# Kernel tuning notes

Measured on AMD Instinct MI355X. Metric: run time of the kernel, lower is better.

Reference implementation:

```python
import jax, jax.numpy as jnp
import numpy as np

D_MODEL = 1024
NUM_HEADS = 16
DEPTH = D_MODEL // NUM_HEADS


def setup_inputs() -> dict:
    key = jax.random.key(0)
    ks = jax.random.split(key, 8)
    B, S, D = 2, 2048, D_MODEL
    s = 1.0 / np.sqrt(D)
    return {
        "q": jax.random.normal(ks[0], (B, S, D), jnp.float32),
        "k": jax.random.normal(ks[1], (B, S, D), jnp.float32),
        "v": jax.random.normal(ks[2], (B, S, D), jnp.float32),
        "Wq": jax.random.normal(ks[3], (D, D), jnp.float32) * s,
        "bq": jnp.zeros((D,), jnp.float32),
        "Wk": jax.random.normal(ks[4], (D, D), jnp.float32) * s,
        "bk": jnp.zeros((D,), jnp.float32),
        "Wv": jax.random.normal(ks[5], (D, D), jnp.float32) * s,
        "bv": jnp.zeros((D,), jnp.float32),
        "Wo": jax.random.normal(ks[6], (D, D), jnp.float32) * s,
        "bo": jnp.zeros((D,), jnp.float32),
    }


def _split_heads(x):
    # [B,S,D] -> [B,H,S,depth]
    B, S, _ = x.shape
    return x.reshape(B, S, NUM_HEADS, DEPTH).transpose(0, 2, 1, 3)


def reference(q, k, v, Wq, bq, Wk, bk, Wv, bv, Wo, bo):
    qh = _split_heads(q @ Wq + bq)  # [B,H,S,d]
    kh = _split_heads(k @ Wk + bk)
    vh = _split_heads(v @ Wv + bv)
    scale = 1.0 / jnp.sqrt(jnp.float32(DEPTH))
    logits = jnp.einsum("bhqd,bhkd->bhqk", qh, kh) * scale  # [B,H,S,S]
    weights = jax.nn.softmax(logits, axis=-1)
    attn = jnp.einsum("bhqk,bhkd->bhqd", weights, vh)
    B, H, S, d = attn.shape
    attn = attn.transpose(0, 2, 1, 3).reshape(B, S, H * d)  # [B,S,D]
    return attn @ Wo + bo
```

## Files before the change

### kernel.cpp

```cpp
#include <hip/hip_runtime.h>
#include <hip/hip_bf16.h>
#include <stdint.h>


typedef __attribute__((ext_vector_type(8))) short bf16x8;
typedef __attribute__((ext_vector_type(4))) float f32x4;

#define MFMA16(a, b, c) __builtin_amdgcn_mfma_f32_16x16x32_bf16((a), (b), (c), 0, 0, 0)
#define EXP2(x) __builtin_amdgcn_exp2f(x)

static constexpr int S_LEN = 2048;
static constexpr int DM    = 1024;
static constexpr int DEPTH = 64;
static constexpr float QSCALE = 0.125f * 1.44269504088896340736f;

__device__ __forceinline__ unsigned short f2b(float f) {
  unsigned u = __float_as_uint(f);
  unsigned r = 0x7FFFu + ((u >> 16) & 1u);
  return (unsigned short)((u + r) >> 16);
}

__device__ __forceinline__ unsigned short b16(float f) {
  __hip_bfloat16 h = __float2bfloat16(f);
  union { __hip_bfloat16 h; unsigned short u; } c; c.h = h; return c.u;
}

__device__ __forceinline__ void gload16(const void* g, void* l) {
  __builtin_amdgcn_global_load_lds(
      (const __attribute__((address_space(1))) void*)g,
      (__attribute__((address_space(3))) void*)l, 16, 0, 0);
}

__device__ __forceinline__ void wave_lds_fence() {
  asm volatile("" ::: "memory");
  __builtin_amdgcn_sched_barrier(0);
}

__global__ __launch_bounds__(256) void prep_k(
    const float* __restrict__ xq, const float* __restrict__ xk,
    const float* __restrict__ xv, unsigned short* __restrict__ Xb,
    const float* __restrict__ Wq, const float* __restrict__ Wk,
    const float* __restrict__ Wv, const float* __restrict__ Wo,
    unsigned short* __restrict__ Wt) {
  __shared__ unsigned short ts[64][68];
  const int bid = blockIdx.x;
  const int tid = threadIdx.x;
  if (bid < 6144) {
    const int which = bid >> 11;
    const int xb = bid & 2047;
    const float* X = (which == 0) ? xq : (which == 1) ? xk : xv;
    size_t gid = ((size_t)xb * 256 + tid) * 8;
    float4 v0 = *(const float4*)&X[gid];
    float4 v1 = *(const float4*)&X[gid + 4];
    union { unsigned short u[8]; bf16x8 v; } pk;
    pk.u[0] = f2b(v0.x); pk.u[1] = f2b(v0.y); pk.u[2] = f2b(v0.z); pk.u[3] = f2b(v0.w);
    pk.u[4] = f2b(v1.x); pk.u[5] = f2b(v1.y); pk.u[6] = f2b(v1.z); pk.u[7] = f2b(v1.w);
    *(bf16x8*)&Xb[(size_t)which * 4096 * DM + gid] = pk.v;
    return;
  }
  const int wb = bid - 6144;
  const int w = wb >> 8, tile = wb & 255;
  const int tr = tile >> 4, tc = tile & 15;
  const float* W = (w == 0) ? Wq : (w == 1) ? Wk : (w == 2) ? Wv : Wo;
  unsigned short* T = Wt + (size_t)w * DM * DM;
  const int kr = tid >> 4, nc = (tid & 15) * 4;
  #pragma unroll
  for (int j = 0; j < 4; ++j) {
    int k = tr * 64 + kr + j * 16;
    float4 v = *(const float4*)&W[(size_t)k * DM + tc * 64 + nc];
    ushort4 u; u.x = f2b(v.x); u.y = f2b(v.y); u.z = f2b(v.z); u.w = f2b(v.w);
    *(ushort4*)&ts[kr + j * 16][nc] = u;
  }
  __syncthreads();
  const int nr = tid >> 4, kc = (tid & 15) * 4;
  #pragma unroll
  for (int j = 0; j < 4; ++j) {
    int n = tc * 64 + nr + j * 16;
    ushort4 u;
    u.x = ts[kc + 0][nr + j * 16];
    u.y = ts[kc + 1][nr + j * 16];
    u.z = ts[kc + 2][nr + j * 16];
    u.w = ts[kc + 3][nr + j * 16];
    *(ushort4*)&T[(size_t)n * DM + tr * 64 + kc] = u;
  }
}

__global__ __launch_bounds__(256, 4) void proj_qkv_k(
    const unsigned short* __restrict__ Xb, const unsigned short* __restrict__ Wt,
    const float* __restrict__ bq, const float* __restrict__ bk, const float* __restrict__ bv,
    unsigned short* __restrict__ Qh, unsigned short* __restrict__ Kh,
    unsigned short* __restrict__ Vt) {
  __shared__ __align__(16) unsigned short As[2][128][32];
  __shared__ __align__(16) unsigned short Bs[2][128][32];

  const int z = blockIdx.z;
  const unsigned short* A  = Xb + (size_t)z * 4096 * DM;
  const unsigned short* Bt = Wt + (size_t)z * DM * DM;
  const float* bias = (z == 0) ? bq : (z == 1) ? bk : bv;
  const float scale = (z == 0) ? QSCALE : 1.0f;
  unsigned short* O = (z == 0) ? Qh : (z == 1) ? Kh : Vt;

  const int bm = blockIdx.x, bn = blockIdx.y;
  const int tid = threadIdx.x;
  const int wave = tid >> 6, lane = tid & 63;
  const int wr = wave >> 1, wc = wave & 1;
  const int g = lane >> 4, i16 = lane & 15;
  const int srow = tid >> 2, sslot = tid & 3;

  f32x4 acc[4][4] = {};

  auto stage = [&](int ks, int buf) {
    #pragma unroll
    for (int rnd = 0; rnd < 2; ++rnd) {
      int row = rnd * 64 + srow;
      int sw = sslot ^ ((row >> 1) & 3);
      gload16(&A[(size_t)(bm * 128 + row) * DM + ks * 32 + sw * 8],
              &As[buf][row][sslot * 8]);
      gload16(&Bt[(size_t)(bn * 128 + row) * DM + ks * 32 + sw * 8],
              &Bs[buf][row][sslot * 8]);
    }
  };
  auto compute = [&](int buf) {
    bf16x8 a[4], b[4];
    #pragma unroll
    for (int m = 0; m < 4; ++m) {
      int row = wr * 64 + m * 16 + i16;
      int sl = g ^ ((row >> 1) & 3);
      a[m] = *(const bf16x8*)&As[buf][row][sl * 8];
    }
    #pragma unroll
    for (int n = 0; n < 4; ++n) {
      int row = wc * 64 + n * 16 + i16;
      int sl = g ^ ((row >> 1) & 3);
      b[n] = *(const bf16x8*)&Bs[buf][row][sl * 8];
    }
    #pragma unroll
    for (int m = 0; m < 4; ++m)
      #pragma unroll
      for (int n = 0; n < 4; ++n)
        acc[m][n] = MFMA16(a[m], b[n], acc[m][n]);
  };

  stage(0, 0);
  __syncthreads();
  int cur = 0;
  #pragma unroll 1
  for (int ks = 0; ks < DM / 32; ++ks) {
    if (ks + 1 < DM / 32) stage(ks + 1, cur ^ 1);
    compute(cur);
    __syncthreads();
    cur ^= 1;
  }

  #pragma unroll
  for (int m = 0; m < 4; ++m) {
    #pragma unroll
    for (int n = 0; n < 4; ++n) {
      #pragma unroll
      for (int r = 0; r < 4; ++r) {
        int row = bm * 128 + wr * 64 + m * 16 + g * 4 + r;
        int col = bn * 128 + wc * 64 + n * 16 + i16;
        float v = (acc[m][n][r] + bias[col]) * scale;
        int b_ = row >> 11, s = row & 2047;
        int h = col >> 6, dd = col & 63;
        if (z != 2)
          O[(((size_t)(b_ * 16 + h)) * S_LEN + s) * DEPTH + dd] = f2b(v);
        else
          O[(((size_t)(b_ * 16 + h)) * DEPTH + dd) * S_LEN + s] = f2b(v);
      }
    }
  }
}

__global__ __launch_bounds__(256, 4) void out_proj_k(
    const unsigned short* __restrict__ At, const unsigned short* __restrict__ Wto,
    const float* __restrict__ bo, float* __restrict__ out) {
  __shared__ __align__(16) unsigned short As[2][64][32];
  __shared__ __align__(16) unsigned short Bs[2][128][32];

  const int bm = blockIdx.x, bn = blockIdx.y;
  const int tid = threadIdx.x;
  const int wave = tid >> 6, lane = tid & 63;
  const int wr = wave >> 1, wc = wave & 1;
  const int g = lane >> 4, i16 = lane & 15;
  const int srow = tid >> 2, sslot = tid & 3;

  f32x4 acc[2][4] = {};

  auto stage = [&](int ks, int buf) {
    {
      int sw = sslot ^ ((srow >> 1) & 3);
      gload16(&At[(size_t)(bm * 64 + srow) * DM + ks * 32 + sw * 8],
              &As[buf][srow][sslot * 8]);
    }
    #pragma unroll
    for (int rnd = 0; rnd < 2; ++rnd) {
      int row = rnd * 64 + srow;
      int sw = sslot ^ ((row >> 1) & 3);
      gload16(&Wto[(size_t)(bn * 128 + row) * DM + ks * 32 + sw * 8],
              &Bs[buf][row][sslot * 8]);
    }
  };
  auto compute = [&](int buf) {
    bf16x8 a[2], b[4];
    #pragma unroll
    for (int m = 0; m < 2; ++m) {
      int row = wr * 32 + m * 16 + i16;
      int sl = g ^ ((row >> 1) & 3);
      a[m] = *(const bf16x8*)&As[buf][row][sl * 8];
    }
    #pragma unroll
    for (int n = 0; n < 4; ++n) {
      int row = wc * 64 + n * 16 + i16;
      int sl = g ^ ((row >> 1) & 3);
      b[n] = *(const bf16x8*)&Bs[buf][row][sl * 8];
    }
    #pragma unroll
    for (int m = 0; m < 2; ++m)
      #pragma unroll
      for (int n = 0; n < 4; ++n)
        acc[m][n] = MFMA16(a[m], b[n], acc[m][n]);
  };

  stage(0, 0);
  __syncthreads();
  int cur = 0;
  #pragma unroll 1
  for (int ks = 0; ks < DM / 32; ++ks) {
    if (ks + 1 < DM / 32) stage(ks + 1, cur ^ 1);
    compute(cur);
    __syncthreads();
    cur ^= 1;
  }

  #pragma unroll
  for (int m = 0; m < 2; ++m) {
    #pragma unroll
    for (int n = 0; n < 4; ++n) {
      #pragma unroll
      for (int r = 0; r < 4; ++r) {
        int row = bm * 64 + wr * 32 + m * 16 + g * 4 + r;
        int col = bn * 128 + wc * 64 + n * 16 + i16;
        out[(size_t)row * DM + col] = acc[m][n][r] + bo[col];
      }
    }
  }
}

__global__ __launch_bounds__(256) void attn_k(
    const unsigned short* __restrict__ Qh, const unsigned short* __restrict__ Kh,
    const unsigned short* __restrict__ Vt, unsigned short* __restrict__ Ob) {
  __shared__ unsigned short Ks[2][128][64];
  __shared__ unsigned short Vs[2][64][128];
  __shared__ unsigned short p_lds[4][2][16][64];

  const int linear = blockIdx.y * 16 + blockIdx.x;
  const int wg = (linear & 7) * 64 + (linear >> 3);
  const int qt = wg & 15, bh = wg >> 4;

  const int tid = threadIdx.x;
  const int wave = tid >> 6, lane = tid & 63;
  const int g = lane >> 4, i16 = lane & 15;

  const unsigned short* Q = Qh + (size_t)bh * S_LEN * DEPTH;
  const unsigned short* K = Kh + (size_t)bh * S_LEN * DEPTH;
  const unsigned short* V = Vt + (size_t)bh * DEPTH * S_LEN;

  const int ksr = tid >> 3, kss = tid & 7;
  const int vsr = tid >> 4, vss = tid & 15;

  const int qbase = qt * 128 + wave * 32;
  bf16x8 qa[2][2];
  #pragma unroll
  for (int qs = 0; qs < 2; ++qs) {
    qa[qs][0] = *(const bf16x8*)&Q[(size_t)(qbase + qs * 16 + i16) * DEPTH + g * 8];
    qa[qs][1] = *(const bf16x8*)&Q[(size_t)(qbase + qs * 16 + i16) * DEPTH + 32 + g * 8];
  }

  const short one_b = (short)0x3F80;
  const bf16x8 ones = {one_b, one_b, one_b, one_b, one_b, one_b, one_b, one_b};

  f32x4 l_acc[2] = {};
  f32x4 o[2][4] = {};

  auto stage = [&](int t, int buf) {
    const int kv = t * 128;
    #pragma unroll
    for (int j = 0; j < 4; ++j) {
      int kr = j * 32 + ksr;
      int ksw = kss ^ (kr & 7);
      gload16(&K[(size_t)(kv + kr) * DEPTH + ksw * 8], &Ks[buf][kr][kss * 8]);
      int vr = j * 16 + vsr;
      int vsw = vss ^ (vr & 7);
      gload16(&V[(size_t)vr * S_LEN + kv + vsw * 8], &Vs[buf][vr][vss * 8]);
    }
  };

  stage(0, 0);
  __syncthreads();

  int cur = 0;
  #pragma unroll 1
  for (int t128 = 0; t128 < 16; ++t128) {
    if (t128 + 1 < 16) stage(t128 + 1, cur ^ 1);

    #pragma unroll
    for (int h = 0; h < 2; ++h) {
      f32x4 sT[2][4];
      const f32x4 zero = {0.f, 0.f, 0.f, 0.f};
      __builtin_amdgcn_s_setprio(1);
      #pragma unroll
      for (int t = 0; t < 4; ++t) {
        int row = h * 64 + t * 16 + i16;
        int x = row & 7;
        bf16x8 k0 = *(const bf16x8*)&Ks[cur][row][(g ^ x) * 8];
        bf16x8 k1 = *(const bf16x8*)&Ks[cur][row][((4 + g) ^ x) * 8];
        #pragma unroll
        for (int qs = 0; qs < 2; ++qs) {
          f32x4 s = MFMA16(k0, qa[qs][0], zero);
          sT[qs][t] = MFMA16(k1, qa[qs][1], s);
        }
      }
      __builtin_amdgcn_s_setprio(0);

      wave_lds_fence();
      #pragma unroll
      for (int qs = 0; qs < 2; ++qs) {
        #pragma unroll
        for (int t = 0; t < 4; ++t) {
          ushort4 w;
          w.x = b16(EXP2(sT[qs][t][0]));
          w.y = b16(EXP2(sT[qs][t][1]));
          w.z = b16(EXP2(sT[qs][t][2]));
          w.w = b16(EXP2(sT[qs][t][3]));
          int idx = (((t * 2 + (g >> 1)) ^ (i16 & 7)) * 8) + (g & 1) * 4;
          *(ushort4*)&p_lds[wave][qs][i16][idx] = w;
        }
      }
      wave_lds_fence();
      bf16x8 pa0[2], pa1[2];
      #pragma unroll
      for (int qs = 0; qs < 2; ++qs) {
        pa0[qs] = *(const bf16x8*)&p_lds[wave][qs][i16][(g ^ (i16 & 7)) * 8];
        pa1[qs] = *(const bf16x8*)&p_lds[wave][qs][i16][((4 + g) ^ (i16 & 7)) * 8];
      }

      __builtin_amdgcn_s_setprio(1);
      #pragma unroll
      for (int dt = 0; dt < 4; ++dt) {
        int row = dt * 16 + i16;
        int x = row & 7;
        bf16x8 v0 = *(const bf16x8*)&Vs[cur][row][((h * 8 + g) ^ x) * 8];
        bf16x8 v1 = *(const bf16x8*)&Vs[cur][row][((h * 8 + 4 + g) ^ x) * 8];
        #pragma unroll
        for (int qs = 0; qs < 2; ++qs) {
          o[qs][dt] = MFMA16(pa0[qs], v0, o[qs][dt]);
          o[qs][dt] = MFMA16(pa1[qs], v1, o[qs][dt]);
        }
      }
      #pragma unroll
      for (int qs = 0; qs < 2; ++qs) {
        l_acc[qs] = MFMA16(pa0[qs], ones, l_acc[qs]);
        l_acc[qs] = MFMA16(pa1[qs], ones, l_acc[qs]);
      }
      __builtin_amdgcn_s_setprio(0);
    }

    __syncthreads();
    cur ^= 1;
  }

  const int b_ = bh >> 4, h_ = bh & 15;
  #pragma unroll
  for (int qs = 0; qs < 2; ++qs) {
    f32x4 rinv;
    #pragma unroll
    for (int r = 0; r < 4; ++r)
      rinv[r] = 1.0f / l_acc[qs][r];
    #pragma unroll
    for (int dt = 0; dt < 4; ++dt) {
      #pragma unroll
      for (int r = 0; r < 4; ++r) {
        int qrow = qbase + qs * 16 + g * 4 + r;
        float val = o[qs][dt][r] * rinv[r];
        Ob[((size_t)(b_ * S_LEN + qrow)) * DM + h_ * DEPTH + dt * 16 + i16] = f2b(val);
      }
    }
  }
}

extern "C" void kernel_launch(void* const* d_in, const int* in_sizes, int n_in,
                              void* d_out, int out_size, void* d_ws, size_t ws_size,
                              hipStream_t stream) {
  const float* q  = (const float*)d_in[0];
  const float* k  = (const float*)d_in[1];
  const float* v  = (const float*)d_in[2];
  const float* Wq = (const float*)d_in[3];
  const float* bq = (const float*)d_in[4];
  const float* Wk = (const float*)d_in[5];
  const float* bk = (const float*)d_in[6];
  const float* Wv = (const float*)d_in[7];
  const float* bv = (const float*)d_in[8];
  const float* Wo = (const float*)d_in[9];
  const float* bo = (const float*)d_in[10];
  float* out = (float*)d_out;

  const size_t HEAD_ELEMS = (size_t)2 * 16 * S_LEN * DEPTH;
  unsigned short* Qh = (unsigned short*)d_ws;
  unsigned short* Kh = Qh + HEAD_ELEMS;
  unsigned short* Vt = Kh + HEAD_ELEMS;
  unsigned short* Xb = Vt + HEAD_ELEMS;
  unsigned short* At = Xb;
  unsigned short* Wt = Xb + 3 * HEAD_ELEMS;

  dim3 blk(256);
  hipLaunchKernelGGL(prep_k, dim3(7168), blk, 0, stream,
                     q, k, v, Xb, Wq, Wk, Wv, Wo, Wt);
  hipLaunchKernelGGL(proj_qkv_k, dim3(32, 8, 3), blk, 0, stream,
                     Xb, Wt, bq, bk, bv, Qh, Kh, Vt);
  hipLaunchKernelGGL(attn_k, dim3(16, 32), blk, 0, stream, Qh, Kh, Vt, At);
  hipLaunchKernelGGL(out_proj_k, dim3(64, 8), blk, 0, stream,
                     At, Wt + (size_t)3 * DM * DM, bo, out);
}
```

Measured before the change: 123.7 us.

## Fuse fp32-to-bf16 activation conversion into QKV projection GEMM loads

```diff
diff --git a/kernel.cpp b/kernel.cpp
--- a/kernel.cpp
+++ b/kernel.cpp
@@ -37,29 +37,13 @@
 }
 
 __global__ __launch_bounds__(256) void prep_k(
-    const float* __restrict__ xq, const float* __restrict__ xk,
-    const float* __restrict__ xv, unsigned short* __restrict__ Xb,
     const float* __restrict__ Wq, const float* __restrict__ Wk,
     const float* __restrict__ Wv, const float* __restrict__ Wo,
     unsigned short* __restrict__ Wt) {
   __shared__ unsigned short ts[64][68];
   const int bid = blockIdx.x;
   const int tid = threadIdx.x;
-  if (bid < 6144) {
-    const int which = bid >> 11;
-    const int xb = bid & 2047;
-    const float* X = (which == 0) ? xq : (which == 1) ? xk : xv;
-    size_t gid = ((size_t)xb * 256 + tid) * 8;
-    float4 v0 = *(const float4*)&X[gid];
-    float4 v1 = *(const float4*)&X[gid + 4];
-    union { unsigned short u[8]; bf16x8 v; } pk;
-    pk.u[0] = f2b(v0.x); pk.u[1] = f2b(v0.y); pk.u[2] = f2b(v0.z); pk.u[3] = f2b(v0.w);
-    pk.u[4] = f2b(v1.x); pk.u[5] = f2b(v1.y); pk.u[6] = f2b(v1.z); pk.u[7] = f2b(v1.w);
-    *(bf16x8*)&Xb[(size_t)which * 4096 * DM + gid] = pk.v;
-    return;
-  }
-  const int wb = bid - 6144;
-  const int w = wb >> 8, tile = wb & 255;
+  const int w = bid >> 8, tile = bid & 255;
   const int tr = tile >> 4, tc = tile & 15;
   const float* W = (w == 0) ? Wq : (w == 1) ? Wk : (w == 2) ? Wv : Wo;
   unsigned short* T = Wt + (size_t)w * DM * DM;
@@ -86,15 +70,16 @@
 }
 
 __global__ __launch_bounds__(256, 4) void proj_qkv_k(
-    const unsigned short* __restrict__ Xb, const unsigned short* __restrict__ Wt,
+    const float* __restrict__ xq, const float* __restrict__ xk,
+    const float* __restrict__ xv, const unsigned short* __restrict__ Wt,
     const float* __restrict__ bq, const float* __restrict__ bk, const float* __restrict__ bv,
     unsigned short* __restrict__ Qh, unsigned short* __restrict__ Kh,
     unsigned short* __restrict__ Vt) {
-  __shared__ __align__(16) unsigned short As[2][128][32];
+  __shared__ __align__(16) float Asf[2][128][32];
   __shared__ __align__(16) unsigned short Bs[2][128][32];
 
   const int z = blockIdx.z;
-  const unsigned short* A  = Xb + (size_t)z * 4096 * DM;
+  const float* A32 = (z == 0) ? xq : (z == 1) ? xk : xv;
   const unsigned short* Bt = Wt + (size_t)z * DM * DM;
   const float* bias = (z == 0) ? bq : (z == 1) ? bk : bv;
   const float scale = (z == 0) ? QSCALE : 1.0f;
@@ -111,11 +96,17 @@
 
   auto stage = [&](int ks, int buf) {
     #pragma unroll
+    for (int j = 0; j < 4; ++j) {
+      int idx = tid + j * 256;
+      int row = idx >> 3, slot = idx & 7;
+      int sw = slot ^ (row & 7);
+      gload16(&A32[(size_t)(bm * 128 + row) * DM + ks * 32 + sw * 4],
+              &Asf[buf][row][slot * 4]);
+    }
+    #pragma unroll
     for (int rnd = 0; rnd < 2; ++rnd) {
       int row = rnd * 64 + srow;
       int sw = sslot ^ ((row >> 1) & 3);
-      gload16(&A[(size_t)(bm * 128 + row) * DM + ks * 32 + sw * 8],
-              &As[buf][row][sslot * 8]);
       gload16(&Bt[(size_t)(bn * 128 + row) * DM + ks * 32 + sw * 8],
               &Bs[buf][row][sslot * 8]);
     }
@@ -125,8 +116,15 @@
     #pragma unroll
     for (int m = 0; m < 4; ++m) {
       int row = wr * 64 + m * 16 + i16;
-      int sl = g ^ ((row >> 1) & 3);
-      a[m] = *(const bf16x8*)&As[buf][row][sl * 8];
+      int x = row & 7;
+      float4 lo = *(const float4*)&Asf[buf][row][((g * 2) ^ x) * 4];
+      float4 hi = *(const float4*)&Asf[buf][row][((g * 2 + 1) ^ x) * 4];
+      union { unsigned short u[8]; bf16x8 v; } pk;
+      pk.u[0] = b16(lo.x); pk.u[1] = b16(lo.y);
+      pk.u[2] = b16(lo.z); pk.u[3] = b16(lo.w);
+      pk.u[4] = b16(hi.x); pk.u[5] = b16(hi.y);
+      pk.u[6] = b16(hi.z); pk.u[7] = b16(hi.w);
+      a[m] = pk.v;
     }
     #pragma unroll
     for (int n = 0; n < 4; ++n) {
@@ -409,15 +407,13 @@
   unsigned short* Qh = (unsigned short*)d_ws;
   unsigned short* Kh = Qh + HEAD_ELEMS;
   unsigned short* Vt = Kh + HEAD_ELEMS;
-  unsigned short* Xb = Vt + HEAD_ELEMS;
-  unsigned short* At = Xb;
-  unsigned short* Wt = Xb + 3 * HEAD_ELEMS;
+  unsigned short* At = Vt + HEAD_ELEMS;
+  unsigned short* Wt = At + 3 * HEAD_ELEMS;
 
   dim3 blk(256);
-  hipLaunchKernelGGL(prep_k, dim3(7168), blk, 0, stream,
-                     q, k, v, Xb, Wq, Wk, Wv, Wo, Wt);
+  hipLaunchKernelGGL(prep_k, dim3(1024), blk, 0, stream, Wq, Wk, Wv, Wo, Wt);
   hipLaunchKernelGGL(proj_qkv_k, dim3(32, 8, 3), blk, 0, stream,
-                     Xb, Wt, bq, bk, bv, Qh, Kh, Vt);
+                     q, k, v, Wt, bq, bk, bv, Qh, Kh, Vt);
   hipLaunchKernelGGL(attn_k, dim3(16, 32), blk, 0, stream, Qh, Kh, Vt, At);
   hipLaunchKernelGGL(out_proj_k, dim3(64, 8), blk, 0, stream,
                      At, Wt + (size_t)3 * DM * DM, bo, out);
```

Measured after the change: 122.1 us, median of 3. Within noise of the previous version (-1.3%).
